# Kernel tuning notes

Measured on AMD Instinct MI355X. Metric: run time of the kernel, lower is better.

Reference implementation:

```python
import jax, jax.numpy as jnp
import numpy as np

N_NODES = 20000
N_EDGES = 320000
N_GRAPHS = 16
NEG_SLOPE = 0.2


def gat_layer(x, src, dst, W, al, ar, b):
    # x: [N, F_in]; W: [F_in, H*D]; al/ar: [H, D]; b: [H*D]
    H, D = al.shape
    N = x.shape[0]
    f = (x @ W).reshape(N, H, D)                      # projected features [N,H,D]
    el = jnp.sum(f * al[None], axis=-1)                # [N,H]
    er = jnp.sum(f * ar[None], axis=-1)                # [N,H]
    e = jax.nn.leaky_relu(el[src] + er[dst], NEG_SLOPE)  # [E,H]
    # numerically stable segment softmax over incoming edges of each dst node
    m = jax.ops.segment_max(e, dst, num_segments=N)    # [N,H]
    m = jnp.where(jnp.isfinite(m), m, 0.0)
    ex = jnp.exp(e - m[dst])                           # [E,H]
    denom = jax.ops.segment_sum(ex, dst, num_segments=N)  # [N,H]
    msg = ex[:, :, None] * f[src]                      # [E,H,D]
    num = jax.ops.segment_sum(msg, dst, num_segments=N)   # [N,H,D]
    rst = num / jnp.where(denom > 0, denom, 1.0)[:, :, None]
    return rst + b.reshape(1, H, D)


def setup_inputs() -> dict:
    key = jax.random.key(0)
    ks = jax.random.split(key, 16)
    in_dim, hid, H = 128, 128, 3
    x = jax.random.normal(ks[0], (N_NODES, in_dim), dtype=jnp.float32)
    src = jax.random.randint(ks[1], (N_EDGES,), 0, N_NODES, dtype=jnp.int32)
    dst = jax.random.randint(ks[2], (N_EDGES,), 0, N_NODES, dtype=jnp.int32)
    graph_ids = jnp.sort(jax.random.randint(ks[3], (N_NODES,), 0, N_GRAPHS, dtype=jnp.int32))
    s = lambda d: 1.0 / np.sqrt(d)
    W1 = jax.random.normal(ks[4], (in_dim, H * hid), jnp.float32) * s(in_dim)
    al1 = jax.random.normal(ks[5], (H, hid), jnp.float32) * s(hid)
    ar1 = jax.random.normal(ks[6], (H, hid), jnp.float32) * s(hid)
    b1 = jnp.zeros((H * hid,), jnp.float32)
    W2 = jax.random.normal(ks[7], (H * hid, hid), jnp.float32) * s(H * hid)
    al2 = jax.random.normal(ks[8], (1, hid), jnp.float32) * s(hid)
    ar2 = jax.random.normal(ks[9], (1, hid), jnp.float32) * s(hid)
    b2 = jnp.zeros((hid,), jnp.float32)
    linW = jax.random.normal(ks[10], (hid, hid), jnp.float32) * s(hid)
    linb = jnp.zeros((hid,), jnp.float32)
    return dict(x=x, src=src, dst=dst, graph_ids=graph_ids, W1=W1, al1=al1,
                ar1=ar1, b1=b1, W2=W2, al2=al2, ar2=ar2, b2=b2, linW=linW, linb=linb)


def reference(x, src, dst, graph_ids, W1, al1, ar1, b1, W2, al2, ar2, b2, linW, linb):
    h = gat_layer(x, src, dst, W1, al1, ar1, b1)       # [N,3,hid]
    h = jax.nn.elu(h.reshape(h.shape[0], -1))          # [N,3*hid]
    h = gat_layer(h, src, dst, W2, al2, ar2, b2)       # [N,1,hid]
    h = h.squeeze(1)                                   # [N,hid]
    # dgl.mean_nodes over batched graph
    sums = jax.ops.segment_sum(h, graph_ids, num_segments=N_GRAPHS)      # [G,hid]
    cnts = jax.ops.segment_sum(jnp.ones_like(graph_ids, jnp.float32), graph_ids, num_segments=N_GRAPHS)
    hg = sums / jnp.maximum(cnts, 1.0)[:, None]
    return jax.nn.relu(hg @ linW + linb)
```

## Files before the change

kernel.cpp:

```cpp
#include <hip/hip_runtime.h>
#include <hip/hip_bf16.h>

#define NN 20000
#define NE 320000
#define NG 16
#define PSPLIT 32
#define NSCANB 79


__global__ void hist_kernel(const int* __restrict__ dst, int* __restrict__ indeg, int E) {
  int e = blockIdx.x * 256 + threadIdx.x;
  if (e < E) atomicAdd(&indeg[dst[e]], 1);
}

__global__ void scan1_kernel(const int* __restrict__ in, int* __restrict__ outp,
                             int* __restrict__ bsum, int n) {
  int b = blockIdx.x, t = threadIdx.x;
  int i = b * 256 + t;
  int lane = t & 63, wv = t >> 6;
  __shared__ int ws[4];
  int v = (i < n) ? in[i] : 0;
  int x = v;
#pragma unroll
  for (int off = 1; off < 64; off <<= 1) {
    int y = __shfl_up(x, off);
    if (lane >= off) x += y;
  }
  if (lane == 63) ws[wv] = x;
  __syncthreads();
  int add = 0;
  for (int w2 = 0; w2 < wv; w2++) add += ws[w2];
  x += add;
  if (i < n) outp[i] = x - v;
  if (t == 255) bsum[b] = x;
}

__global__ void scan2_kernel(const int* __restrict__ bsum, int* __restrict__ boff,
                             int* __restrict__ rp_end, int nb) {
  int t = threadIdx.x;
  int lane = t & 63, wv = t >> 6;
  __shared__ int ws[2];
  int v = (t < nb) ? bsum[t] : 0;
  int x = v;
#pragma unroll
  for (int off = 1; off < 64; off <<= 1) {
    int y = __shfl_up(x, off);
    if (lane >= off) x += y;
  }
  if (lane == 63) ws[wv] = x;
  __syncthreads();
  if (wv == 1) x += ws[0];
  if (t < nb) boff[t] = x - v;
  if (t == 127) *rp_end = x;
}

__global__ void scan3_kernel(int* __restrict__ outp, const int* __restrict__ boff, int n) {
  int i = blockIdx.x * 256 + threadIdx.x;
  if (i < n) outp[i] += boff[blockIdx.x];
}

__global__ void scatter_kernel(const int* __restrict__ src, const int* __restrict__ dst,
                               const int* __restrict__ rowptr, int* __restrict__ cursor,
                               int* __restrict__ csr_src, int E) {
  int e = blockIdx.x * 256 + threadIdx.x;
  if (e < E) {
    int d = dst[e];
    int p = atomicAdd(&cursor[d], 1);
    csr_src[rowptr[d] + p] = src[e];
  }
}


__global__ void prep_wlr_kernel(const float* __restrict__ W1, const float* __restrict__ al1,
                                const float* __restrict__ ar1, float* __restrict__ wlr) {
  int t = blockIdx.x * 256 + threadIdx.x;
  if (t >= 768) return;
  int k = t & 127;
  int j = t >> 7;
  int h = j % 3;
  const float* av = (j < 3 ? al1 : ar1) + h * 128;
  const float* wrow = W1 + (size_t)k * 384 + h * 128;
  float s = 0.f;
#pragma unroll 4
  for (int d = 0; d < 128; d++) s += wrow[d] * av[d];
  wlr[j * 128 + k] = s;
}

__global__ void elr_kernel(const float* __restrict__ x, const float* __restrict__ wlr,
                           float* __restrict__ el, float* __restrict__ er, int N) {
  __shared__ float wl_s[768];
  int t = threadIdx.x;
  for (int i = t; i < 768; i += 256) wl_s[i] = wlr[i];
  __syncthreads();
  int w = (blockIdx.x * 256 + t) >> 6;
  int lane = t & 63;
  if (w >= N) return;
  float v0 = x[(size_t)w * 128 + lane], v1 = x[(size_t)w * 128 + 64 + lane];
  float s[6];
#pragma unroll
  for (int j = 0; j < 6; j++) s[j] = v0 * wl_s[j * 128 + lane] + v1 * wl_s[j * 128 + 64 + lane];
#pragma unroll
  for (int off = 32; off; off >>= 1)
#pragma unroll
    for (int j = 0; j < 6; j++) s[j] += __shfl_down(s[j], off);
  if (lane == 0) {
    el[w * 3 + 0] = s[0]; el[w * 3 + 1] = s[1]; el[w * 3 + 2] = s[2];
    er[w * 3 + 0] = s[3]; er[w * 3 + 1] = s[4]; er[w * 3 + 2] = s[5];
  }
}


__global__ void aggregate_x_kernel(const float* __restrict__ x, const float* __restrict__ el,
                                   const float* __restrict__ er, const int* __restrict__ rowptr,
                                   const int* __restrict__ csr_src, float* __restrict__ aggx) {
  int n = blockIdx.x;
  int t = threadIdx.x;
  __shared__ float wbuf[3][128];
  __shared__ int sbuf[128];
  __shared__ float red[6];
  __shared__ float4 accbuf[3][4][32];
  int rs = rowptr[n];
  int deg = rowptr[n + 1] - rs;
  float er0 = er[n * 3 + 0], er1 = er[n * 3 + 1], er2 = er[n * 3 + 2];
  float p0 = 0.f, p1 = 0.f, p2 = 0.f;
  int g = t >> 5, dq = t & 31;
  const float* xd = x + dq * 4;
  float4 a0 = make_float4(0, 0, 0, 0), a1 = a0, a2 = a0;
  for (int base = 0; base < deg; base += 128) {
    int cnt = min(128, deg - base);
    if (t < cnt) {
      int s = csr_src[rs + base + t];
      sbuf[t] = s;
      float e0 = el[s * 3 + 0] + er0, e1 = el[s * 3 + 1] + er1, e2 = el[s * 3 + 2] + er2;
      e0 = e0 > 0.f ? e0 : 0.2f * e0;
      e1 = e1 > 0.f ? e1 : 0.2f * e1;
      e2 = e2 > 0.f ? e2 : 0.2f * e2;
      float w0 = __expf(e0), w1 = __expf(e1), w2 = __expf(e2);
      wbuf[0][t] = w0; wbuf[1][t] = w1; wbuf[2][t] = w2;
      p0 += w0; p1 += w1; p2 += w2;
    }
    __syncthreads();
    int j = g;
    for (; j + 4 < cnt; j += 8) {
      int s0 = sbuf[j], s1 = sbuf[j + 4];
      float4 v0 = *(const float4*)(xd + (size_t)s0 * 128);
      float4 v1 = *(const float4*)(xd + (size_t)s1 * 128);
      float w00 = wbuf[0][j], w01 = wbuf[1][j], w02 = wbuf[2][j];
      float w10 = wbuf[0][j + 4], w11 = wbuf[1][j + 4], w12 = wbuf[2][j + 4];
      a0.x += w00 * v0.x + w10 * v1.x; a0.y += w00 * v0.y + w10 * v1.y;
      a0.z += w00 * v0.z + w10 * v1.z; a0.w += w00 * v0.w + w10 * v1.w;
      a1.x += w01 * v0.x + w11 * v1.x; a1.y += w01 * v0.y + w11 * v1.y;
      a1.z += w01 * v0.z + w11 * v1.z; a1.w += w01 * v0.w + w11 * v1.w;
      a2.x += w02 * v0.x + w12 * v1.x; a2.y += w02 * v0.y + w12 * v1.y;
      a2.z += w02 * v0.z + w12 * v1.z; a2.w += w02 * v0.w + w12 * v1.w;
    }
    for (; j < cnt; j += 4) {
      int s = sbuf[j];
      float4 v = *(const float4*)(xd + (size_t)s * 128);
      float w0 = wbuf[0][j], w1 = wbuf[1][j], w2 = wbuf[2][j];
      a0.x += w0 * v.x; a0.y += w0 * v.y; a0.z += w0 * v.z; a0.w += w0 * v.w;
      a1.x += w1 * v.x; a1.y += w1 * v.y; a1.z += w1 * v.z; a1.w += w1 * v.w;
      a2.x += w2 * v.x; a2.y += w2 * v.y; a2.z += w2 * v.z; a2.w += w2 * v.w;
    }
    __syncthreads();
  }
  for (int off = 32; off; off >>= 1) {
    p0 += __shfl_down(p0, off);
    p1 += __shfl_down(p1, off);
    p2 += __shfl_down(p2, off);
  }
  int wv = t >> 6, ln = t & 63;
  if (ln == 0) { red[wv * 3 + 0] = p0; red[wv * 3 + 1] = p1; red[wv * 3 + 2] = p2; }
  accbuf[0][g][dq] = a0;
  accbuf[1][g][dq] = a1;
  accbuf[2][g][dq] = a2;
  __syncthreads();
  if (t < 96) {
    int h = t >> 5, d = t & 31;
    float4 s0 = accbuf[h][0][d], s1 = accbuf[h][1][d], s2 = accbuf[h][2][d], s3 = accbuf[h][3][d];
    float dn = red[h] + red[3 + h];
    float inv = dn > 0.f ? 1.f / dn : 0.f;
    float4 r;
    r.x = (s0.x + s1.x + s2.x + s3.x) * inv;
    r.y = (s0.y + s1.y + s2.y + s3.y) * inv;
    r.z = (s0.z + s1.z + s2.z + s3.z) * inv;
    r.w = (s0.w + s1.w + s2.w + s3.w) * inv;
    *(float4*)&aggx[(size_t)n * 384 + h * 128 + d * 4] = r;
  }
}


template <int K, bool HEADS, bool BIAS_ELU>
__launch_bounds__(128)
__global__ void gemm3264_kernel(const float* __restrict__ A, int lda,
                                const float* __restrict__ B, int ldb,
                                float* __restrict__ C, int ldc,
                                const float* __restrict__ bias) {
  __shared__ float As[32 * 40];
  __shared__ float Bs[32 * 64];
  int t = threadIdx.x;
  int m0 = blockIdx.x * 32;
  int col0 = blockIdx.y * 64;
  if (HEADS) A += (size_t)(col0 >> 7) * 128;
  int tm = t >> 4, tn = t & 15;
  float acc[4][4];
#pragma unroll
  for (int i = 0; i < 4; i++)
#pragma unroll
    for (int j = 0; j < 4; j++) acc[i][j] = 0.f;

  for (int k0 = 0; k0 < K; k0 += 32) {
#pragma unroll
    for (int i = 0; i < 2; i++) {
      int idx = t + i * 128;
      int r = idx >> 3, kq = (idx & 7) * 4;
      float4 v = *(const float4*)&A[(size_t)(m0 + r) * lda + k0 + kq];
      As[(kq + 0) * 40 + r] = v.x;
      As[(kq + 1) * 40 + r] = v.y;
      As[(kq + 2) * 40 + r] = v.z;
      As[(kq + 3) * 40 + r] = v.w;
    }
#pragma unroll
    for (int i = 0; i < 4; i++) {
      int idx = t + i * 128;
      int kk = idx >> 4, nq = (idx & 15) * 4;
      *(float4*)&Bs[kk * 64 + nq] = *(const float4*)&B[(size_t)(k0 + kk) * ldb + col0 + nq];
    }
    __syncthreads();
#pragma unroll
    for (int k = 0; k < 32; k++) {
      float4 a = *(const float4*)&As[k * 40 + tm * 4];
      float4 b = *(const float4*)&Bs[k * 64 + tn * 4];
      float af[4] = {a.x, a.y, a.z, a.w};
      float bf[4] = {b.x, b.y, b.z, b.w};
#pragma unroll
      for (int i = 0; i < 4; i++)
#pragma unroll
        for (int j = 0; j < 4; j++) acc[i][j] += af[i] * bf[j];
    }
    __syncthreads();
  }
  float bv[4];
  if (BIAS_ELU) {
#pragma unroll
    for (int j = 0; j < 4; j++) bv[j] = bias[col0 + tn * 4 + j];
  }
#pragma unroll
  for (int i = 0; i < 4; i++) {
    int gm = m0 + tm * 4 + i;
    float r[4];
#pragma unroll
    for (int j = 0; j < 4; j++) {
      float v = acc[i][j];
      if (BIAS_ELU) {
        v += bv[j];
        v = v > 0.f ? v : expm1f(v);
      }
      r[j] = v;
    }
    *(float4*)&C[(size_t)gm * ldc + col0 + tn * 4] = make_float4(r[0], r[1], r[2], r[3]);
  }
}


__global__ void att_coef_kernel(const float* __restrict__ f, const float* __restrict__ al,
                                const float* __restrict__ ar, float* __restrict__ el,
                                float* __restrict__ er, int NH) {
  int w = (blockIdx.x * 256 + threadIdx.x) >> 6;
  int lane = threadIdx.x & 63;
  if (w >= NH) return;
  const float* fr = f + (size_t)w * 128;
  float v0 = fr[lane], v1 = fr[64 + lane];
  float a0 = al[lane], a1 = al[64 + lane];
  float r0 = ar[lane], r1 = ar[64 + lane];
  float se = v0 * a0 + v1 * a1;
  float sr = v0 * r0 + v1 * r1;
  for (int off = 32; off; off >>= 1) {
    se += __shfl_down(se, off);
    sr += __shfl_down(sr, off);
  }
  if (lane == 0) { el[w] = se; er[w] = sr; }
}


__global__ void aggregate1_kernel(const float* __restrict__ f, const float* __restrict__ el,
                                  const float* __restrict__ er, const float* __restrict__ bias,
                                  const int* __restrict__ rowptr, const int* __restrict__ csr_src,
                                  float* __restrict__ out) {
  int n = blockIdx.x;
  int t = threadIdx.x;
  __shared__ float wbuf[128];
  __shared__ int sbuf[128];
  __shared__ float red[2];
  __shared__ float4 accbuf[4][32];
  int rs = rowptr[n];
  int deg = rowptr[n + 1] - rs;
  float ern = er[n];
  float psum = 0.f;
  int g = t >> 5;
  int d = (t & 31) * 4;
  const float* fd = f + d;
  float4 acc = make_float4(0.f, 0.f, 0.f, 0.f);
  for (int base = 0; base < deg; base += 128) {
    int cnt = min(128, deg - base);
    if (t < cnt) {
      int s = csr_src[rs + base + t];
      sbuf[t] = s;
      float e = el[s] + ern;
      e = e > 0.f ? e : 0.2f * e;
      float w = __expf(e);
      wbuf[t] = w;
      psum += w;
    }
    __syncthreads();
    int j = g;
    for (; j + 4 < cnt; j += 8) {
      int s0 = sbuf[j], s1 = sbuf[j + 4];
      float4 v0 = *(const float4*)(fd + (size_t)s0 * 128);
      float4 v1 = *(const float4*)(fd + (size_t)s1 * 128);
      float w0 = wbuf[j], w1 = wbuf[j + 4];
      acc.x += w0 * v0.x + w1 * v1.x;
      acc.y += w0 * v0.y + w1 * v1.y;
      acc.z += w0 * v0.z + w1 * v1.z;
      acc.w += w0 * v0.w + w1 * v1.w;
    }
    for (; j < cnt; j += 4) {
      int s = sbuf[j];
      float4 v = *(const float4*)(fd + (size_t)s * 128);
      float w = wbuf[j];
      acc.x += w * v.x; acc.y += w * v.y; acc.z += w * v.z; acc.w += w * v.w;
    }
    __syncthreads();
  }
  for (int off = 32; off; off >>= 1) psum += __shfl_down(psum, off);
  int wv = t >> 6, ln = t & 63;
  if (ln == 0) red[wv] = psum;
  accbuf[g][t & 31] = acc;
  __syncthreads();
  if (t < 32) {
    float4 a0 = accbuf[0][t], a1 = accbuf[1][t], a2 = accbuf[2][t], a3 = accbuf[3][t];
    float dn = red[0] + red[1];
    float inv = dn > 0.f ? 1.f / dn : 0.f;
    const float* bp = bias + t * 4;
    float4 r;
    r.x = (a0.x + a1.x + a2.x + a3.x) * inv + bp[0];
    r.y = (a0.y + a1.y + a2.y + a3.y) * inv + bp[1];
    r.z = (a0.z + a1.z + a2.z + a3.z) * inv + bp[2];
    r.w = (a0.w + a1.w + a2.w + a3.w) * inv + bp[3];
    *(float4*)&out[(size_t)n * 128 + t * 4] = r;
  }
}


__global__ void pool_partial_kernel(const float* __restrict__ h2, const int* __restrict__ gid,
                                    float* __restrict__ sums, int N) {
  int g = blockIdx.x / PSPLIT;
  int sp = blockIdx.x % PSPLIT;
  int tid = threadIdx.x;
  int lo0 = 0, hi0 = N;
  while (lo0 < hi0) { int m = (lo0 + hi0) >> 1; if (gid[m] < g) lo0 = m + 1; else hi0 = m; }
  int lo1 = lo0, hi1 = N;
  while (lo1 < hi1) { int m = (lo1 + hi1) >> 1; if (gid[m] < g + 1) lo1 = m + 1; else hi1 = m; }
  float a0 = 0.f, a1 = 0.f, a2 = 0.f, a3 = 0.f;
  int n = lo0 + sp;
  for (; n + 3 * PSPLIT < lo1; n += 4 * PSPLIT) {
    a0 += h2[(size_t)n * 128 + tid];
    a1 += h2[(size_t)(n + PSPLIT) * 128 + tid];
    a2 += h2[(size_t)(n + 2 * PSPLIT) * 128 + tid];
    a3 += h2[(size_t)(n + 3 * PSPLIT) * 128 + tid];
  }
  for (; n < lo1; n += PSPLIT) a0 += h2[(size_t)n * 128 + tid];
  float acc = (a0 + a1) + (a2 + a3);
  atomicAdd(&sums[g * 128 + tid], acc);
}

__global__ void pool_final_kernel(const float* __restrict__ sums, const int* __restrict__ gid,
                                  const float* __restrict__ linW, const float* __restrict__ linb,
                                  float* __restrict__ out, int N) {
  int g = blockIdx.x;
  int tid = threadIdx.x;
  int lo0 = 0, hi0 = N;
  while (lo0 < hi0) { int m = (lo0 + hi0) >> 1; if (gid[m] < g) lo0 = m + 1; else hi0 = m; }
  int lo1 = lo0, hi1 = N;
  while (lo1 < hi1) { int m = (lo1 + hi1) >> 1; if (gid[m] < g + 1) lo1 = m + 1; else hi1 = m; }
  int cnt = lo1 - lo0;
  float hg = sums[g * 128 + tid] / (float)(cnt > 0 ? cnt : 1);
  __shared__ float hgs[128];
  hgs[tid] = hg;
  __syncthreads();
  float o = linb[tid];
#pragma unroll 4
  for (int dd = 0; dd < 128; dd++) o += hgs[dd] * linW[dd * 128 + tid];
  out[g * 128 + tid] = fmaxf(o, 0.f);
}


extern "C" void kernel_launch(void* const* d_in, const int* in_sizes, int n_in,
                              void* d_out, int out_size, void* d_ws, size_t ws_size,
                              hipStream_t stream) {
  const float* x    = (const float*)d_in[0];
  const int*   src  = (const int*)d_in[1];
  const int*   dst  = (const int*)d_in[2];
  const int*   gid  = (const int*)d_in[3];
  const float* W1   = (const float*)d_in[4];
  const float* al1  = (const float*)d_in[5];
  const float* ar1  = (const float*)d_in[6];
  const float* b1   = (const float*)d_in[7];
  const float* W2   = (const float*)d_in[8];
  const float* al2  = (const float*)d_in[9];
  const float* ar2  = (const float*)d_in[10];
  const float* b2   = (const float*)d_in[11];
  const float* linW = (const float*)d_in[12];
  const float* linb = (const float*)d_in[13];
  float* out = (float*)d_out;

  char* ws = (char*)d_ws;
  size_t off = 0;
  auto alloc = [&](size_t bytes) -> void* {
    void* p = ws + off;
    off += (bytes + 255) & ~(size_t)255;
    return p;
  };
  float* aggx    = (float*)alloc((size_t)NN * 384 * 4);
  float* h1      = (float*)alloc((size_t)NN * 384 * 4);
  float* f2      = (float*)alloc((size_t)NN * 128 * 4);
  float* h2      = (float*)alloc((size_t)NN * 128 * 4);
  float* el1     = (float*)alloc((size_t)NN * 3 * 4);
  float* er1     = (float*)alloc((size_t)NN * 3 * 4);
  float* el2     = (float*)alloc((size_t)NN * 4);
  float* er2     = (float*)alloc((size_t)NN * 4);
  float* wlr     = (float*)alloc((size_t)768 * 4);
  int*   rowptr  = (int*)alloc((size_t)(NN + 1) * 4);
  int*   csr_src = (int*)alloc((size_t)NE * 4);
  int*   bsum    = (int*)alloc((size_t)NSCANB * 4);
  int*   boff    = (int*)alloc((size_t)NSCANB * 4);
  int*   indeg   = (int*)alloc((size_t)NN * 4);
  int*   cursor  = (int*)alloc((size_t)NN * 4);
  float* gsums   = (float*)alloc((size_t)NG * 128 * 4);
  (void)ws_size;
  size_t zbytes = (char*)(gsums + NG * 128) - (char*)indeg;
  hipMemsetAsync(indeg, 0, zbytes, stream);

  hist_kernel<<<(NE + 255) / 256, 256, 0, stream>>>(dst, indeg, NE);
  scan1_kernel<<<NSCANB, 256, 0, stream>>>(indeg, rowptr, bsum, NN);
  scan2_kernel<<<1, 128, 0, stream>>>(bsum, boff, rowptr + NN, NSCANB);
  scan3_kernel<<<NSCANB, 256, 0, stream>>>(rowptr, boff, NN);
  scatter_kernel<<<(NE + 255) / 256, 256, 0, stream>>>(src, dst, rowptr, cursor, csr_src, NE);

  prep_wlr_kernel<<<3, 256, 0, stream>>>(W1, al1, ar1, wlr);
  elr_kernel<<<(NN + 3) / 4, 256, 0, stream>>>(x, wlr, el1, er1, NN);
  aggregate_x_kernel<<<NN, 128, 0, stream>>>(x, el1, er1, rowptr, csr_src, aggx);
  gemm3264_kernel<128, true, true><<<dim3(625, 6), 128, 0, stream>>>(
      aggx, 384, W1, 384, h1, 384, b1);

  gemm3264_kernel<384, false, false><<<dim3(625, 2), 128, 0, stream>>>(
      h1, 384, W2, 128, f2, 128, nullptr);
  att_coef_kernel<<<(NN + 3) / 4, 256, 0, stream>>>(f2, al2, ar2, el2, er2, NN);
  aggregate1_kernel<<<NN, 128, 0, stream>>>(f2, el2, er2, b2, rowptr, csr_src, h2);

  pool_partial_kernel<<<NG * PSPLIT, 128, 0, stream>>>(h2, gid, gsums, NN);
  pool_final_kernel<<<NG, 128, 0, stream>>>(gsums, gid, linW, linb, out, NN);
}
```

Before: 290.5 us.

## Pack preprocessing kernels into fewer launches and restructure GEMM to stream B from global

Independent preprocessing kernels are merged by block-index partitioning: histogram with the attention-weight precompute, scan1 with the el/er computation, and the scatter with the scan offset fix-up, which removes scan3 and cuts the launch count. The GEMM no longer stages B in shared memory; each thread reads an 8-wide B row slice directly from global/cache and uses an R x 8 register tile with a narrower A pad. The layer-1 GEMM now covers 128 columns per block, one head per block. The aim is less launch overhead and less shared-memory staging, at the cost of more global loads of B per thread.

After: 368.0 us. +26.7%, slower.

```diff
diff --git a/kernel.cpp b/kernel.cpp
--- a/kernel.cpp
+++ b/kernel.cpp
@@ -6,33 +6,74 @@
 #define NG 16
 #define PSPLIT 32
 #define NSCANB 79
-
-
-__global__ void hist_kernel(const int* __restrict__ dst, int* __restrict__ indeg, int E) {
-  int e = blockIdx.x * 256 + threadIdx.x;
-  if (e < E) atomicAdd(&indeg[dst[e]], 1);
-}
-
-__global__ void scan1_kernel(const int* __restrict__ in, int* __restrict__ outp,
-                             int* __restrict__ bsum, int n) {
+#define NHISTB 1250
+
+
+__global__ void pack_hist_wlr_kernel(const int* __restrict__ dst, int* __restrict__ indeg,
+                                     const float* __restrict__ W1, const float* __restrict__ al1,
+                                     const float* __restrict__ ar1, float* __restrict__ wlr) {
   int b = blockIdx.x, t = threadIdx.x;
-  int i = b * 256 + t;
+  if (b < NHISTB) {
+    int e = b * 256 + t;
+    if (e < NE) atomicAdd(&indeg[dst[e]], 1);
+  } else {
+    int idx = (b - NHISTB) * 256 + t;
+    if (idx >= 768) return;
+    int k = idx & 127;
+    int j = idx >> 7;
+    int h = j % 3;
+    const float* av = (j < 3 ? al1 : ar1) + h * 128;
+    const float* wrow = W1 + (size_t)k * 384 + h * 128;
+    float s = 0.f;
+#pragma unroll 4
+    for (int d = 0; d < 128; d++) s += wrow[d] * av[d];
+    wlr[j * 128 + k] = s;
+  }
+}
+
+
+__global__ void pack_scan1_elr_kernel(const int* __restrict__ indeg, int* __restrict__ loc,
+                                      int* __restrict__ bsum, const float* __restrict__ x,
+                                      const float* __restrict__ wlr, float* __restrict__ el,
+                                      float* __restrict__ er) {
+  __shared__ int ws[4];
+  __shared__ float wl_s[768];
+  int b = blockIdx.x, t = threadIdx.x;
   int lane = t & 63, wv = t >> 6;
-  __shared__ int ws[4];
-  int v = (i < n) ? in[i] : 0;
-  int x = v;
-#pragma unroll
-  for (int off = 1; off < 64; off <<= 1) {
-    int y = __shfl_up(x, off);
-    if (lane >= off) x += y;
-  }
-  if (lane == 63) ws[wv] = x;
-  __syncthreads();
-  int add = 0;
-  for (int w2 = 0; w2 < wv; w2++) add += ws[w2];
-  x += add;
-  if (i < n) outp[i] = x - v;
-  if (t == 255) bsum[b] = x;
+  if (b < NSCANB) {
+    int i = b * 256 + t;
+    int v = (i < NN) ? indeg[i] : 0;
+    int xx = v;
+#pragma unroll
+    for (int off = 1; off < 64; off <<= 1) {
+      int y = __shfl_up(xx, off);
+      if (lane >= off) xx += y;
+    }
+    if (lane == 63) ws[wv] = xx;
+    __syncthreads();
+    int add = 0;
+    for (int w2 = 0; w2 < wv; w2++) add += ws[w2];
+    xx += add;
+    if (i < NN) loc[i] = xx - v;
+    if (t == 255) bsum[b] = xx;
+  } else {
+    for (int i = t; i < 768; i += 256) wl_s[i] = wlr[i];
+    __syncthreads();
+    int w = ((b - NSCANB) * 256 + t) >> 6;
+    if (w >= NN) return;
+    float v0 = x[(size_t)w * 128 + lane], v1 = x[(size_t)w * 128 + 64 + lane];
+    float s[6];
+#pragma unroll
+    for (int j = 0; j < 6; j++) s[j] = v0 * wl_s[j * 128 + lane] + v1 * wl_s[j * 128 + 64 + lane];
+#pragma unroll
+    for (int off = 32; off; off >>= 1)
+#pragma unroll
+      for (int j = 0; j < 6; j++) s[j] += __shfl_down(s[j], off);
+    if (lane == 0) {
+      el[w * 3 + 0] = s[0]; el[w * 3 + 1] = s[1]; el[w * 3 + 2] = s[2];
+      er[w * 3 + 0] = s[3]; er[w * 3 + 1] = s[4]; er[w * 3 + 2] = s[5];
+    }
+  }
 }
 
 __global__ void scan2_kernel(const int* __restrict__ bsum, int* __restrict__ boff,
@@ -54,58 +95,22 @@
   if (t == 127) *rp_end = x;
 }
 
-__global__ void scan3_kernel(int* __restrict__ outp, const int* __restrict__ boff, int n) {
-  int i = blockIdx.x * 256 + threadIdx.x;
-  if (i < n) outp[i] += boff[blockIdx.x];
-}
-
-__global__ void scatter_kernel(const int* __restrict__ src, const int* __restrict__ dst,
-                               const int* __restrict__ rowptr, int* __restrict__ cursor,
-                               int* __restrict__ csr_src, int E) {
-  int e = blockIdx.x * 256 + threadIdx.x;
-  if (e < E) {
-    int d = dst[e];
-    int p = atomicAdd(&cursor[d], 1);
-    csr_src[rowptr[d] + p] = src[e];
-  }
-}
-
-
-__global__ void prep_wlr_kernel(const float* __restrict__ W1, const float* __restrict__ al1,
-                                const float* __restrict__ ar1, float* __restrict__ wlr) {
-  int t = blockIdx.x * 256 + threadIdx.x;
-  if (t >= 768) return;
-  int k = t & 127;
-  int j = t >> 7;
-  int h = j % 3;
-  const float* av = (j < 3 ? al1 : ar1) + h * 128;
-  const float* wrow = W1 + (size_t)k * 384 + h * 128;
-  float s = 0.f;
-#pragma unroll 4
-  for (int d = 0; d < 128; d++) s += wrow[d] * av[d];
-  wlr[j * 128 + k] = s;
-}
-
-__global__ void elr_kernel(const float* __restrict__ x, const float* __restrict__ wlr,
-                           float* __restrict__ el, float* __restrict__ er, int N) {
-  __shared__ float wl_s[768];
-  int t = threadIdx.x;
-  for (int i = t; i < 768; i += 256) wl_s[i] = wlr[i];
-  __syncthreads();
-  int w = (blockIdx.x * 256 + t) >> 6;
-  int lane = t & 63;
-  if (w >= N) return;
-  float v0 = x[(size_t)w * 128 + lane], v1 = x[(size_t)w * 128 + 64 + lane];
-  float s[6];
-#pragma unroll
-  for (int j = 0; j < 6; j++) s[j] = v0 * wl_s[j * 128 + lane] + v1 * wl_s[j * 128 + 64 + lane];
-#pragma unroll
-  for (int off = 32; off; off >>= 1)
-#pragma unroll
-    for (int j = 0; j < 6; j++) s[j] += __shfl_down(s[j], off);
-  if (lane == 0) {
-    el[w * 3 + 0] = s[0]; el[w * 3 + 1] = s[1]; el[w * 3 + 2] = s[2];
-    er[w * 3 + 0] = s[3]; er[w * 3 + 1] = s[4]; er[w * 3 + 2] = s[5];
+
+__global__ void pack_scatter_fin_kernel(const int* __restrict__ src, const int* __restrict__ dst,
+                                        const int* __restrict__ loc, const int* __restrict__ boff,
+                                        int* __restrict__ cursor, int* __restrict__ csr_src,
+                                        int* __restrict__ rowptr) {
+  int b = blockIdx.x, t = threadIdx.x;
+  if (b < NHISTB) {
+    int e = b * 256 + t;
+    if (e < NE) {
+      int d = dst[e];
+      int p = atomicAdd(&cursor[d], 1);
+      csr_src[loc[d] + boff[d >> 8] + p] = src[e];
+    }
+  } else {
+    int i = (b - NHISTB) * 256 + t;
+    if (i < NN) rowptr[i] = loc[i] + boff[i >> 8];
   }
 }
 
@@ -190,24 +195,26 @@
 }
 
 
-template <int K, bool HEADS, bool BIAS_ELU>
+template <int K, int R, bool HEADS, bool BIAS_ELU>
 __launch_bounds__(128)
-__global__ void gemm3264_kernel(const float* __restrict__ A, int lda,
-                                const float* __restrict__ B, int ldb,
-                                float* __restrict__ C, int ldc,
-                                const float* __restrict__ bias) {
-  __shared__ float As[32 * 40];
-  __shared__ float Bs[32 * 64];
+__global__ void gemm_bg_kernel(const float* __restrict__ A, int lda,
+                               const float* __restrict__ B, int ldb,
+                               float* __restrict__ C, int ldc,
+                               const float* __restrict__ bias) {
+  __shared__ float As[32 * 36];
+  constexpr int TM = 32 / R;
   int t = threadIdx.x;
   int m0 = blockIdx.x * 32;
-  int col0 = blockIdx.y * 64;
-  if (HEADS) A += (size_t)(col0 >> 7) * 128;
-  int tm = t >> 4, tn = t & 15;
-  float acc[4][4];
-#pragma unroll
-  for (int i = 0; i < 4; i++)
-#pragma unroll
-    for (int j = 0; j < 4; j++) acc[i][j] = 0.f;
+  int col0 = blockIdx.y * (32 * R);
+  if (HEADS) A += col0;
+  int tm = t / (128 / TM);
+  int tn = t % (128 / TM);
+  const float* Bp = B + col0 + tn * 8;
+  float acc[R][8];
+#pragma unroll
+  for (int i = 0; i < R; i++)
+#pragma unroll
+    for (int j = 0; j < 8; j++) acc[i][j] = 0.f;
 
   for (int k0 = 0; k0 < K; k0 += 32) {
 #pragma unroll
@@ -215,42 +222,39 @@
       int idx = t + i * 128;
       int r = idx >> 3, kq = (idx & 7) * 4;
       float4 v = *(const float4*)&A[(size_t)(m0 + r) * lda + k0 + kq];
-      As[(kq + 0) * 40 + r] = v.x;
-      As[(kq + 1) * 40 + r] = v.y;
-      As[(kq + 2) * 40 + r] = v.z;
-      As[(kq + 3) * 40 + r] = v.w;
-    }
-#pragma unroll
-    for (int i = 0; i < 4; i++) {
-      int idx = t + i * 128;
-      int kk = idx >> 4, nq = (idx & 15) * 4;
-      *(float4*)&Bs[kk * 64 + nq] = *(const float4*)&B[(size_t)(k0 + kk) * ldb + col0 + nq];
-    }
-    __syncthreads();
-#pragma unroll
+      As[(kq + 0) * 36 + r] = v.x;
+      As[(kq + 1) * 36 + r] = v.y;
+      As[(kq + 2) * 36 + r] = v.z;
+      As[(kq + 3) * 36 + r] = v.w;
+    }
+    __syncthreads();
+#pragma unroll 8
     for (int k = 0; k < 32; k++) {
-      float4 a = *(const float4*)&As[k * 40 + tm * 4];
-      float4 b = *(const float4*)&Bs[k * 64 + tn * 4];
-      float af[4] = {a.x, a.y, a.z, a.w};
-      float bf[4] = {b.x, b.y, b.z, b.w};
-#pragma unroll
-      for (int i = 0; i < 4; i++)
-#pragma unroll
-        for (int j = 0; j < 4; j++) acc[i][j] += af[i] * bf[j];
-    }
-    __syncthreads();
-  }
-  float bv[4];
+      const float* brow = Bp + (size_t)(k0 + k) * ldb;
+      float4 b0 = *(const float4*)brow;
+      float4 b1 = *(const float4*)(brow + 4);
+      float bf[8] = {b0.x, b0.y, b0.z, b0.w, b1.x, b1.y, b1.z, b1.w};
+      float af[R];
+#pragma unroll
+      for (int i = 0; i < R; i++) af[i] = As[k * 36 + tm * R + i];
+#pragma unroll
+      for (int i = 0; i < R; i++)
+#pragma unroll
+        for (int j = 0; j < 8; j++) acc[i][j] += af[i] * bf[j];
+    }
+    __syncthreads();
+  }
+  float bv[8];
   if (BIAS_ELU) {
 #pragma unroll
-    for (int j = 0; j < 4; j++) bv[j] = bias[col0 + tn * 4 + j];
-  }
-#pragma unroll
-  for (int i = 0; i < 4; i++) {
-    int gm = m0 + tm * 4 + i;
-    float r[4];
-#pragma unroll
-    for (int j = 0; j < 4; j++) {
+    for (int j = 0; j < 8; j++) bv[j] = bias[col0 + tn * 8 + j];
+  }
+#pragma unroll
+  for (int i = 0; i < R; i++) {
+    int gm = m0 + tm * R + i;
+    float r[8];
+#pragma unroll
+    for (int j = 0; j < 8; j++) {
       float v = acc[i][j];
       if (BIAS_ELU) {
         v += bv[j];
@@ -258,7 +262,8 @@
       }
       r[j] = v;
     }
-    *(float4*)&C[(size_t)gm * ldc + col0 + tn * 4] = make_float4(r[0], r[1], r[2], r[3]);
+    *(float4*)&C[(size_t)gm * ldc + col0 + tn * 8] = make_float4(r[0], r[1], r[2], r[3]);
+    *(float4*)&C[(size_t)gm * ldc + col0 + tn * 8 + 4] = make_float4(r[4], r[5], r[6], r[7]);
   }
 }
 
@@ -430,6 +435,7 @@
   float* el2     = (float*)alloc((size_t)NN * 4);
   float* er2     = (float*)alloc((size_t)NN * 4);
   float* wlr     = (float*)alloc((size_t)768 * 4);
+  int*   loc     = (int*)alloc((size_t)NN * 4);
   int*   rowptr  = (int*)alloc((size_t)(NN + 1) * 4);
   int*   csr_src = (int*)alloc((size_t)NE * 4);
   int*   bsum    = (int*)alloc((size_t)NSCANB * 4);
@@ -441,21 +447,19 @@
   size_t zbytes = (char*)(gsums + NG * 128) - (char*)indeg;
   hipMemsetAsync(indeg, 0, zbytes, stream);
 
-  hist_kernel<<<(NE + 255) / 256, 256, 0, stream>>>(dst, indeg, NE);
-  scan1_kernel<<<NSCANB, 256, 0, stream>>>(indeg, rowptr, bsum, NN);
+  pack_hist_wlr_kernel<<<NHISTB + 3, 256, 0, stream>>>(dst, indeg, W1, al1, ar1, wlr);
+  pack_scan1_elr_kernel<<<NSCANB + 5000, 256, 0, stream>>>(indeg, loc, bsum, x, wlr, el1, er1);
   scan2_kernel<<<1, 128, 0, stream>>>(bsum, boff, rowptr + NN, NSCANB);
-  scan3_kernel<<<NSCANB, 256, 0, stream>>>(rowptr, boff, NN);
-  scatter_kernel<<<(NE + 255) / 256, 256, 0, stream>>>(src, dst, rowptr, cursor, csr_src, NE);
-
-  prep_wlr_kernel<<<3, 256, 0, stream>>>(W1, al1, ar1, wlr);
-  elr_kernel<<<(NN + 3) / 4, 256, 0, stream>>>(x, wlr, el1, er1, NN);
+  pack_scatter_fin_kernel<<<NHISTB + NSCANB, 256, 0, stream>>>(src, dst, loc, boff, cursor,
+                                                               csr_src, rowptr);
+
   aggregate_x_kernel<<<NN, 128, 0, stream>>>(x, el1, er1, rowptr, csr_src, aggx);
-  gemm3264_kernel<128, true, true><<<dim3(625, 6), 128, 0, stream>>>(
+  gemm_bg_kernel<128, 4, true, true><<<dim3(625, 3), 128, 0, stream>>>(
       aggx, 384, W1, 384, h1, 384, b1);
 
-  gemm3264_kernel<384, false, false><<<dim3(625, 2), 128, 0, stream>>>(
+  gemm_bg_kernel<384, 2, false, false><<<dim3(625, 2), 128, 0, stream>>>(
       h1, 384, W2, 128, f2, 128, nullptr);
-  att_coef_kernel<<<(NN + 3) / 4, 256, 0, stream>>>(f2, al2, ar2, el2, er2, NN);
+  att_coef_kernel<<<5000, 256, 0, stream>>>(f2, al2, ar2, el2, er2, NN);
   aggregate1_kernel<<<NN, 128, 0, stream>>>(f2, el2, er2, b2, rowptr, csr_src, h2);
 
   pool_partial_kernel<<<NG * PSPLIT, 128, 0, stream>>>(h2, gid, gsums, NN);
```
